# Performance work log

Measured on AMD Instinct MI355X. Metric: run time of the kernel, lower is better.

Reference implementation:

```python
import jax, jax.numpy as jnp
import numpy as np

B, S, D = 2, 2048, 1024
H = 16
DK = D // H  # 64
THETA = 10000.0
CLAMP = 80.0


def setup_inputs() -> dict:
    key = jax.random.key(0)
    ks = jax.random.split(key, 5)
    scale = 1.0 / np.sqrt(D)
    return {
        "x": jax.random.normal(ks[0], (B, S, D), jnp.float32),
        "Wq": jax.random.normal(ks[1], (D, D), jnp.float32) * scale,
        "Wk": jax.random.normal(ks[2], (D, D), jnp.float32) * scale,
        "Wv": jax.random.normal(ks[3], (D, D), jnp.float32) * scale,
        "Wo": jax.random.normal(ks[4], (D, D), jnp.float32) * scale,
    }


def _rope(x):
    # x: (B, H, S, DK); rotate interleaved even/odd pairs
    pos = jnp.arange(S, dtype=jnp.float32)  # token_positions = arange
    inv_freq = 1.0 / (THETA ** (jnp.arange(0, DK, 2, dtype=jnp.float32) / DK))
    ang = pos[:, None] * inv_freq[None, :]  # (S, DK/2)
    cos, sin = jnp.cos(ang), jnp.sin(ang)
    x1, x2 = x[..., 0::2], x[..., 1::2]
    r1 = x1 * cos - x2 * sin
    r2 = x1 * sin + x2 * cos
    out = jnp.stack([r1, r2], axis=-1).reshape(x.shape)
    return out


def reference(x, Wq, Wk, Wv, Wo):
    # fused-style QKV projections (bias-free Linear: y = x @ W^T)
    def proj(W):
        y = jnp.einsum('bsd,ed->bse', x, W)
        return y.reshape(B, S, H, DK).transpose(0, 2, 1, 3)  # b h s dk
    Q, K, V = proj(Wq), proj(Wk), proj(Wv)
    Q, K = _rope(Q), _rope(K)
    # naive attention with score clamp then causal mask then scaled softmax
    scores = jnp.einsum('bhqd,bhkd->bhqk', Q, K)
    scores = jnp.clip(scores, -CLAMP, CLAMP)
    causal = jnp.tril(jnp.ones((S, S), dtype=bool))  # (q, k)
    scores = jnp.where(causal, scores, -jnp.inf)
    weights = jax.nn.softmax(scores / np.sqrt(DK), axis=-1)
    att = jnp.einsum('bhqk,bhkd->bhqd', weights, V)
    att = att.transpose(0, 2, 1, 3).reshape(B, S, D)
    return jnp.einsum('bsd,ed->bse', att, Wo)
```

## Files before the change

### kernel.cpp

```cpp
#include <hip/hip_runtime.h>
#include <hip/hip_bf16.h>

#define Bc 2
#define Sc 2048
#define Dc 1024
#define Hc 16
#define DKc 64
#define Mrows 4096
#define QKV_LD 3072

typedef __bf16 bf16;
typedef __bf16 bf16x8 __attribute__((ext_vector_type(8)));
typedef __bf16 bf16x4 __attribute__((ext_vector_type(4)));
typedef float f32x4 __attribute__((ext_vector_type(4)));

__global__ void cvt_f32_bf16(const float* __restrict__ in, bf16* __restrict__ out, int n) {
    int idx = (blockIdx.x * blockDim.x + threadIdx.x) * 4;
    if (idx < n) {
        float4 v = *(const float4*)(in + idx);
        bf16x4 o = { (bf16)v.x, (bf16)v.y, (bf16)v.z, (bf16)v.w };
        *(bf16x4*)(out + idx) = o;
    }
}

__global__ void cvt_w4(const float* __restrict__ a, const float* __restrict__ b,
                       const float* __restrict__ c, const float* __restrict__ d,
                       bf16* __restrict__ oa, bf16* __restrict__ ob,
                       bf16* __restrict__ oc, bf16* __restrict__ od) {
    int idx = (blockIdx.x * blockDim.x + threadIdx.x) * 4;
    const float* in; bf16* out;
    switch (blockIdx.y) {
        case 0: in = a; out = oa; break;
        case 1: in = b; out = ob; break;
        case 2: in = c; out = oc; break;
        default: in = d; out = od; break;
    }
    float4 v = *(const float4*)(in + idx);
    bf16x4 o = { (bf16)v.x, (bf16)v.y, (bf16)v.z, (bf16)v.w };
    *(bf16x4*)(out + idx) = o;
}

__device__ __forceinline__ void gld_lds16(const bf16* g, bf16* l) {
    __builtin_amdgcn_global_load_lds((const __attribute__((address_space(1))) void*)g,
                                     (__attribute__((address_space(3))) void*)l, 16, 0, 0);
}

__device__ __forceinline__ unsigned bperm(int addrBytes, unsigned v) {
    return (unsigned)__builtin_amdgcn_ds_bpermute(addrBytes, (int)v);
}

template <typename OutT>
__global__ __launch_bounds__(512) void gemm_bt(const bf16* __restrict__ A,
                                               const bf16* __restrict__ Bt,
                                               OutT* __restrict__ C,
                                               int M, int N, int K) {
    __shared__ bf16 As[128 * 64];
    __shared__ bf16 Bs[128 * 64];
    const int tid = threadIdx.x;
    const int bm = blockIdx.y * 128, bn = blockIdx.x * 128;
    const int w = tid >> 6, l = tid & 63;
    const int wr = w >> 2, wc = w & 3;
    const int lr = l & 15, lc = l >> 4;

    const int srow = l >> 3;
    const int gl = (l & 7) ^ srow;
    const bf16* Ag = A  + (size_t)(bm + w * 16 + srow) * K + gl * 8;
    const bf16* Bg = Bt + (size_t)(bn + w * 16 + srow) * K + gl * 8;

    f32x4 acc[4][2] = {};

    for (int k0 = 0; k0 < K; k0 += 64) {
        __syncthreads();
#pragma unroll
        for (int c = 0; c < 2; c++) {
            gld_lds16(Ag + (size_t)(c * 8) * K + k0, &As[(w * 16 + c * 8) * 64]);
            gld_lds16(Bg + (size_t)(c * 8) * K + k0, &Bs[(w * 16 + c * 8) * 64]);
        }
        __syncthreads();
#pragma unroll
        for (int s = 0; s < 2; s++) {
            bf16x8 af[4], bfr[2];
#pragma unroll
            for (int i = 0; i < 4; i++) {
                const int R = wr * 64 + i * 16 + lr;
                af[i] = *(bf16x8*)&As[R * 64 + (((s * 4 + lc) ^ (R & 7)) * 8)];
            }
#pragma unroll
            for (int j = 0; j < 2; j++) {
                const int R = wc * 32 + j * 16 + lr;
                bfr[j] = *(bf16x8*)&Bs[R * 64 + (((s * 4 + lc) ^ (R & 7)) * 8)];
            }
#pragma unroll
            for (int i = 0; i < 4; i++)
#pragma unroll
                for (int j = 0; j < 2; j++)
                    acc[i][j] = __builtin_amdgcn_mfma_f32_16x16x32_bf16(af[i], bfr[j], acc[i][j], 0, 0, 0);
        }
    }

    const int cr = (l >> 4) * 4, cc = l & 15;
#pragma unroll
    for (int i = 0; i < 4; i++)
#pragma unroll
        for (int j = 0; j < 2; j++)
#pragma unroll
            for (int r = 0; r < 4; r++) {
                int row = bm + wr * 64 + i * 16 + cr + r;
                int col = bn + wc * 32 + j * 16 + cc;
                C[(size_t)row * N + col] = (OutT)acc[i][j][r];
            }
}

__global__ void rope_k(bf16* __restrict__ QKV) {
    int i = blockIdx.x * blockDim.x + threadIdx.x;
    int pair = i & 31;
    int h = (i >> 5) & 15;
    int s = (i >> 9) & 2047;
    int b = i >> 20;
    float inv_freq = exp2f(-0.41524101186f * (float)pair);
    float ang = (float)s * inv_freq;
    float c = cosf(ang), sn = sinf(ang);
    size_t base = ((size_t)(b * Sc + s)) * QKV_LD + h * 64 + pair * 2;
    float q1 = (float)QKV[base], q2 = (float)QKV[base + 1];
    QKV[base]     = (bf16)(q1 * c - q2 * sn);
    QKV[base + 1] = (bf16)(q1 * sn + q2 * c);
    size_t kb = base + 1024;
    float k1 = (float)QKV[kb], k2 = (float)QKV[kb + 1];
    QKV[kb]     = (bf16)(k1 * c - k2 * sn);
    QKV[kb + 1] = (bf16)(k1 * sn + k2 * c);
}

__global__ __launch_bounds__(256) void vtrans(const bf16* __restrict__ QKV, bf16* __restrict__ Vt) {
    __shared__ bf16 T[64 * 68];
    const int s0 = blockIdx.x * 64;
    const int bh = blockIdx.y;
    const int b = bh >> 4, h = bh & 15;
    const int tid = threadIdx.x;
    const bf16* src = QKV + (size_t)(b * Sc + s0) * QKV_LD + 2048 + h * 64;
#pragma unroll
    for (int p = 0; p < 2; p++) {
        int sr = (tid >> 3) + p * 32;
        int dk0 = (tid & 7) * 8;
        bf16x8 v = *(const bf16x8*)(src + (size_t)sr * QKV_LD + dk0);
        bf16x4 lo = { v[0], v[1], v[2], v[3] }, hi = { v[4], v[5], v[6], v[7] };
        *(bf16x4*)&T[sr * 68 + dk0]     = lo;
        *(bf16x4*)&T[sr * 68 + dk0 + 4] = hi;
    }
    __syncthreads();
    bf16* dst = Vt + (size_t)(bh * 64) * Sc + s0;
#pragma unroll
    for (int p = 0; p < 2; p++) {
        int dk = (tid >> 3) + p * 32;
        int sc0 = (tid & 7) * 8;
        bf16x8 v;
#pragma unroll
        for (int e = 0; e < 8; e++) v[e] = T[(sc0 + e) * 68 + dk];
        *(bf16x8*)(dst + (size_t)dk * Sc + sc0) = v;
    }
}

__global__ __launch_bounds__(256) void attn_k(const bf16* __restrict__ QKV,
                                              const bf16* __restrict__ Vt,
                                              bf16* __restrict__ Oa) {
    __shared__ bf16 Ks[2][64 * 64];
    __shared__ bf16 Vs[2][64 * 64];

    const int bid = blockIdx.x;
    const int qi = 31 - (bid >> 5);
    const int bh = bid & 31;
    const int h = bh & 15, b = bh >> 4;
    const int q0 = qi * 64;
    const int tid = threadIdx.x, w = tid >> 6, l = tid & 63;
    const int lr = l & 15, lc = l >> 4;

    const bf16* Qb  = QKV + (size_t)(b * Sc) * QKV_LD + h * 64;
    const bf16* Kb  = QKV + (size_t)(b * Sc) * QKV_LD + 1024 + h * 64;
    const bf16* Vtb = Vt + (size_t)(bh * 64) * Sc;

    const int qrow = q0 + w * 16 + lr;
    bf16x8 qf0 = *(const bf16x8*)(Qb + (size_t)qrow * QKV_LD + lc * 8);
    bf16x8 qf1 = *(const bf16x8*)(Qb + (size_t)qrow * QKV_LD + 32 + lc * 8);

    const int r8 = l >> 3, glg = (l & 7) ^ r8;
    const bf16* Kg = Kb  + (size_t)(16 * w + r8) * QKV_LD + glg * 8;
    const bf16* Vg = Vtb + (size_t)(16 * w + r8) * Sc + glg * 8;

    f32x4 oacc[4] = {};
    float psum = 0.f;

    const int sA = (lr + ((lc & 1) << 5)) << 2;
    const int sB = sA + (16 << 2);
    const bool hij = (lc & 2) != 0;

    const int nt = qi + 1;
    int cur = 0;

#define STAGE(T, BUF) {                                                            \
    const size_t kof = (size_t)((T) * 64) * QKV_LD;                                \
    const size_t vof = (size_t)((T) * 64);                                         \
    gld_lds16(Kg + kof,                    &Ks[BUF][(16 * w) * 64]);               \
    gld_lds16(Kg + kof + (size_t)8 * QKV_LD, &Ks[BUF][(16 * w + 8) * 64]);         \
    gld_lds16(Vg + vof,                    &Vs[BUF][(16 * w) * 64]);               \
    gld_lds16(Vg + vof + (size_t)8 * Sc,   &Vs[BUF][(16 * w + 8) * 64]); }

    STAGE(0, 0);
    for (int t = 0; t < nt; t++) {
        const int k0 = t * 64;
        if (t + 1 < nt) {
            __builtin_amdgcn_s_barrier();
            STAGE(t + 1, cur ^ 1);
            asm volatile("s_waitcnt vmcnt(4)" ::: "memory");
        } else {
            asm volatile("s_waitcnt vmcnt(0)" ::: "memory");
        }
        __builtin_amdgcn_s_barrier();

        f32x4 sfr[4];
#pragma unroll
        for (int j = 0; j < 4; j++) {
            const int R = j * 16 + lr;
            bf16x8 kf0 = *(bf16x8*)&Ks[cur][R * 64 + ((lc ^ (lr & 7)) * 8)];
            bf16x8 kf1 = *(bf16x8*)&Ks[cur][R * 64 + (((4 + lc) ^ (lr & 7)) * 8)];
            f32x4 z = {};
            z = __builtin_amdgcn_mfma_f32_16x16x32_bf16(kf0, qf0, z, 0, 0, 0);
            z = __builtin_amdgcn_mfma_f32_16x16x32_bf16(kf1, qf1, z, 0, 0, 0);
            sfr[j] = z;
        }

        const bool diag = (t == nt - 1);
        const int qg = q0 + w * 16 + lr;
        float pv[4][4];
#pragma unroll
        for (int j = 0; j < 4; j++)
#pragma unroll
            for (int r = 0; r < 4; r++) {
                float s = fminf(fmaxf(sfr[j][r], -80.f), 80.f);
                float p = __expf(s * 0.125f - 10.0f);
                if (diag && (k0 + j * 16 + lc * 4 + r) > qg) p = 0.f;
                psum += p;
                pv[j][r] = p;
            }

        unsigned pw0[4], pw1[4];
#pragma unroll
        for (int j = 0; j < 4; j++) {
            asm("v_cvt_pk_bf16_f32 %0, %1, %2" : "=v"(pw0[j]) : "v"(pv[j][0]), "v"(pv[j][1]));
            asm("v_cvt_pk_bf16_f32 %0, %1, %2" : "=v"(pw1[j]) : "v"(pv[j][2]), "v"(pv[j][3]));
        }

        union { int4 i; bf16x8 h; } u0, u1;
        {
            unsigned t0 = bperm(sA, pw0[0]), s0_ = bperm(sA, pw0[1]);
            unsigned t1 = bperm(sA, pw1[0]), s1_ = bperm(sA, pw1[1]);
            unsigned t2 = bperm(sB, pw0[0]), s2_ = bperm(sB, pw0[1]);
            unsigned t3 = bperm(sB, pw1[0]), s3_ = bperm(sB, pw1[1]);
            u0.i = (int4){ (int)(hij ? s0_ : t0), (int)(hij ? s1_ : t1),
                           (int)(hij ? s2_ : t2), (int)(hij ? s3_ : t3) };
            unsigned v0 = bperm(sA, pw0[2]), r0_ = bperm(sA, pw0[3]);
            unsigned v1 = bperm(sA, pw1[2]), r1_ = bperm(sA, pw1[3]);
            unsigned v2 = bperm(sB, pw0[2]), r2_ = bperm(sB, pw0[3]);
            unsigned v3 = bperm(sB, pw1[2]), r3_ = bperm(sB, pw1[3]);
            u1.i = (int4){ (int)(hij ? r0_ : v0), (int)(hij ? r1_ : v1),
                           (int)(hij ? r2_ : v2), (int)(hij ? r3_ : v3) };
        }

#pragma unroll
        for (int jd = 0; jd < 4; jd++) {
            const int R = jd * 16 + lr;
            bf16x8 vf0 = *(bf16x8*)&Vs[cur][R * 64 + ((lc ^ (lr & 7)) * 8)];
            bf16x8 vf1 = *(bf16x8*)&Vs[cur][R * 64 + (((4 + lc) ^ (lr & 7)) * 8)];
            oacc[jd] = __builtin_amdgcn_mfma_f32_16x16x32_bf16(u0.h, vf0, oacc[jd], 0, 0, 0);
            oacc[jd] = __builtin_amdgcn_mfma_f32_16x16x32_bf16(u1.h, vf1, oacc[jd], 0, 0, 0);
        }
        cur ^= 1;
    }

    psum += __shfl_xor(psum, 16, 64);
    psum += __shfl_xor(psum, 32, 64);
    float pr[4];
#pragma unroll
    for (int r = 0; r < 4; r++) pr[r] = __shfl(psum, lc * 4 + r, 64);

    bf16* Ob = Oa + (size_t)(b * Sc) * Dc + h * 64;
#pragma unroll
    for (int jd = 0; jd < 4; jd++)
#pragma unroll
        for (int r = 0; r < 4; r++) {
            int qg2 = q0 + w * 16 + lc * 4 + r;
            Ob[(size_t)qg2 * Dc + jd * 16 + lr] = (bf16)(oacc[jd][r] / pr[r]);
        }
#undef STAGE
}

extern "C" void kernel_launch(void* const* d_in, const int* in_sizes, int n_in,
                              void* d_out, int out_size, void* d_ws, size_t ws_size,
                              hipStream_t stream) {
    const float* x  = (const float*)d_in[0];
    const float* Wq = (const float*)d_in[1];
    const float* Wk = (const float*)d_in[2];
    const float* Wv = (const float*)d_in[3];
    const float* Wo = (const float*)d_in[4];

    const int NX = Bc * Sc * Dc;
    const int NW = Dc * Dc;

    bf16* xb   = (bf16*)d_ws;
    bf16* wqb  = xb + NX;
    bf16* wkb  = wqb + NW;
    bf16* wvb  = wkb + NW;
    bf16* wob  = wvb + NW;
    bf16* QKV  = wob + NW;
    bf16* Vt   = QKV + (size_t)Mrows * QKV_LD;
    bf16* att  = xb;

    cvt_f32_bf16<<<NX / 4 / 256, 256, 0, stream>>>(x, xb, NX);
    cvt_w4<<<dim3(NW / 4 / 256, 4), 256, 0, stream>>>(Wq, Wk, Wv, Wo, wqb, wkb, wvb, wob);

    gemm_bt<bf16><<<dim3(QKV_LD / 128, Mrows / 128), 512, 0, stream>>>(xb, wqb, QKV, Mrows, QKV_LD, Dc);

    rope_k<<<(Bc * Sc * Hc * 32) / 256, 256, 0, stream>>>(QKV);
    vtrans<<<dim3(Sc / 64, Bc * Hc), 256, 0, stream>>>(QKV, Vt);

    attn_k<<<Bc * Hc * (Sc / 64), 256, 0, stream>>>(QKV, Vt, att);

    gemm_bt<float><<<dim3(Dc / 128, Mrows / 128), 512, 0, stream>>>(att, wob, (float*)d_out, Mrows, Dc, Dc);
}
```

Baseline: 188.2 us.

## Pair high and low causal query tiles per block to balance attention work

Each attention block now handles two query tiles, tile p and tile 31-p, so every block does the same amount of causal work (33 KV tiles). KV tiles shared by both query tiles are loaded into LDS once and reused for both. The grid is halved to 512 blocks and each block holds two sets of accumulators, which raises register pressure and gives fewer blocks to hide latency with. The aim is to remove the load imbalance from the triangular causal mask and cut redundant K/V loads.

Result: slower. 197.4 us (+4.9%).

```diff
diff --git a/kernel.cpp b/kernel.cpp
--- a/kernel.cpp
+++ b/kernel.cpp
@@ -159,6 +159,88 @@
     }
 }
 
+__device__ __forceinline__ f32x4 mfma16(bf16x8 a, bf16x8 b, f32x4 c) {
+    return __builtin_amdgcn_mfma_f32_16x16x32_bf16(a, b, c, 0, 0, 0);
+}
+
+__device__ __forceinline__ void smax_exch(const f32x4* sfr, int k0, int qg, bool diag,
+                                          int lr, int lc, int sA, int sB, bool hij,
+                                          float& psum, bf16x8& a0, bf16x8& a1) {
+    float pv[4][4];
+#pragma unroll
+    for (int j = 0; j < 4; j++)
+#pragma unroll
+        for (int r = 0; r < 4; r++) {
+            float s = fminf(fmaxf(sfr[j][r], -80.f), 80.f);
+            float p = __expf(s * 0.125f - 10.0f);
+            if (diag && (k0 + j * 16 + lc * 4 + r) > qg) p = 0.f;
+            psum += p;
+            pv[j][r] = p;
+        }
+    unsigned pw0[4], pw1[4];
+#pragma unroll
+    for (int j = 0; j < 4; j++) {
+        asm("v_cvt_pk_bf16_f32 %0, %1, %2" : "=v"(pw0[j]) : "v"(pv[j][0]), "v"(pv[j][1]));
+        asm("v_cvt_pk_bf16_f32 %0, %1, %2" : "=v"(pw1[j]) : "v"(pv[j][2]), "v"(pv[j][3]));
+    }
+    union { int4 i; bf16x8 h; } u0, u1;
+    {
+        unsigned t0 = bperm(sA, pw0[0]), s0_ = bperm(sA, pw0[1]);
+        unsigned t1 = bperm(sA, pw1[0]), s1_ = bperm(sA, pw1[1]);
+        unsigned t2 = bperm(sB, pw0[0]), s2_ = bperm(sB, pw0[1]);
+        unsigned t3 = bperm(sB, pw1[0]), s3_ = bperm(sB, pw1[1]);
+        u0.i = (int4){ (int)(hij ? s0_ : t0), (int)(hij ? s1_ : t1),
+                       (int)(hij ? s2_ : t2), (int)(hij ? s3_ : t3) };
+        unsigned v0 = bperm(sA, pw0[2]), r0_ = bperm(sA, pw0[3]);
+        unsigned v1 = bperm(sA, pw1[2]), r1_ = bperm(sA, pw1[3]);
+        unsigned v2 = bperm(sB, pw0[2]), r2_ = bperm(sB, pw0[3]);
+        unsigned v3 = bperm(sB, pw1[2]), r3_ = bperm(sB, pw1[3]);
+        u1.i = (int4){ (int)(hij ? r0_ : v0), (int)(hij ? r1_ : v1),
+                       (int)(hij ? r2_ : v2), (int)(hij ? r3_ : v3) };
+    }
+    a0 = u0.h; a1 = u1.h;
+}
+
+template <bool DOL>
+__device__ __forceinline__ void attn_tile(const bf16* Ksb, const bf16* Vsb,
+                                          int lr, int lc, int k0,
+                                          bf16x8 qHf0, bf16x8 qHf1, bf16x8 qLf0, bf16x8 qLf1,
+                                          int qgH, int qgL, bool diagH, bool diagL,
+                                          int sA, int sB, bool hij,
+                                          f32x4* oH, f32x4* oL, float& psH, float& psL) {
+    f32x4 sH[4], sL[4];
+#pragma unroll
+    for (int j = 0; j < 4; j++) {
+        const int R = j * 16 + lr;
+        bf16x8 kf0 = *(bf16x8*)&Ksb[R * 64 + ((lc ^ (lr & 7)) * 8)];
+        bf16x8 kf1 = *(bf16x8*)&Ksb[R * 64 + (((4 + lc) ^ (lr & 7)) * 8)];
+        f32x4 z = {};
+        z = mfma16(kf0, qHf0, z); z = mfma16(kf1, qHf1, z);
+        sH[j] = z;
+        if constexpr (DOL) {
+            f32x4 y = {};
+            y = mfma16(kf0, qLf0, y); y = mfma16(kf1, qLf1, y);
+            sL[j] = y;
+        }
+    }
+    bf16x8 aH0, aH1, aL0, aL1;
+    smax_exch(sH, k0, qgH, diagH, lr, lc, sA, sB, hij, psH, aH0, aH1);
+    if constexpr (DOL) smax_exch(sL, k0, qgL, diagL, lr, lc, sA, sB, hij, psL, aL0, aL1);
+
+#pragma unroll
+    for (int jd = 0; jd < 4; jd++) {
+        const int R = jd * 16 + lr;
+        bf16x8 vf0 = *(bf16x8*)&Vsb[R * 64 + ((lc ^ (lr & 7)) * 8)];
+        bf16x8 vf1 = *(bf16x8*)&Vsb[R * 64 + (((4 + lc) ^ (lr & 7)) * 8)];
+        oH[jd] = mfma16(aH0, vf0, oH[jd]);
+        oH[jd] = mfma16(aH1, vf1, oH[jd]);
+        if constexpr (DOL) {
+            oL[jd] = mfma16(aL0, vf0, oL[jd]);
+            oL[jd] = mfma16(aL1, vf1, oL[jd]);
+        }
+    }
+}
+
 __global__ __launch_bounds__(256) void attn_k(const bf16* __restrict__ QKV,
                                               const bf16* __restrict__ Vt,
                                               bf16* __restrict__ Oa) {
@@ -166,10 +248,10 @@
     __shared__ bf16 Vs[2][64 * 64];
 
     const int bid = blockIdx.x;
-    const int qi = 31 - (bid >> 5);
+    const int p = bid >> 5;
     const int bh = bid & 31;
     const int h = bh & 15, b = bh >> 4;
-    const int q0 = qi * 64;
+    const int qHt = 31 - p, qLt = p;
     const int tid = threadIdx.x, w = tid >> 6, l = tid & 63;
     const int lr = l & 15, lc = l >> 4;
 
@@ -177,119 +259,99 @@
     const bf16* Kb  = QKV + (size_t)(b * Sc) * QKV_LD + 1024 + h * 64;
     const bf16* Vtb = Vt + (size_t)(bh * 64) * Sc;
 
-    const int qrow = q0 + w * 16 + lr;
-    bf16x8 qf0 = *(const bf16x8*)(Qb + (size_t)qrow * QKV_LD + lc * 8);
-    bf16x8 qf1 = *(const bf16x8*)(Qb + (size_t)qrow * QKV_LD + 32 + lc * 8);
+    const int qrowH = qHt * 64 + w * 16 + lr;
+    const int qrowL = qLt * 64 + w * 16 + lr;
+    bf16x8 qHf0 = *(const bf16x8*)(Qb + (size_t)qrowH * QKV_LD + lc * 8);
+    bf16x8 qHf1 = *(const bf16x8*)(Qb + (size_t)qrowH * QKV_LD + 32 + lc * 8);
+    bf16x8 qLf0 = *(const bf16x8*)(Qb + (size_t)qrowL * QKV_LD + lc * 8);
+    bf16x8 qLf1 = *(const bf16x8*)(Qb + (size_t)qrowL * QKV_LD + 32 + lc * 8);
 
     const int r8 = l >> 3, glg = (l & 7) ^ r8;
     const bf16* Kg = Kb  + (size_t)(16 * w + r8) * QKV_LD + glg * 8;
     const bf16* Vg = Vtb + (size_t)(16 * w + r8) * Sc + glg * 8;
 
-    f32x4 oacc[4] = {};
-    float psum = 0.f;
+    f32x4 oH[4] = {}, oL[4] = {};
+    float psH = 0.f, psL = 0.f;
 
     const int sA = (lr + ((lc & 1) << 5)) << 2;
     const int sB = sA + (16 << 2);
     const bool hij = (lc & 2) != 0;
 
-    const int nt = qi + 1;
+    const int qgH = qHt * 64 + w * 16 + lr;
+    const int qgL = qLt * 64 + w * 16 + lr;
+
+    const int nt = qHt + 1;
     int cur = 0;
 
 #define STAGE(T, BUF) {                                                            \
     const size_t kof = (size_t)((T) * 64) * QKV_LD;                                \
     const size_t vof = (size_t)((T) * 64);                                         \
-    gld_lds16(Kg + kof,                    &Ks[BUF][(16 * w) * 64]);               \
+    gld_lds16(Kg + kof,                      &Ks[BUF][(16 * w) * 64]);             \
     gld_lds16(Kg + kof + (size_t)8 * QKV_LD, &Ks[BUF][(16 * w + 8) * 64]);         \
-    gld_lds16(Vg + vof,                    &Vs[BUF][(16 * w) * 64]);               \
-    gld_lds16(Vg + vof + (size_t)8 * Sc,   &Vs[BUF][(16 * w + 8) * 64]); }
+    gld_lds16(Vg + vof,                      &Vs[BUF][(16 * w) * 64]);             \
+    gld_lds16(Vg + vof + (size_t)8 * Sc,     &Vs[BUF][(16 * w + 8) * 64]); }
 
     STAGE(0, 0);
-    for (int t = 0; t < nt; t++) {
-        const int k0 = t * 64;
+    for (int t = 0; t <= p; t++) {
+        __builtin_amdgcn_s_barrier();
+        STAGE(t + 1, cur ^ 1);
+        asm volatile("s_waitcnt vmcnt(4)" ::: "memory");
+        __builtin_amdgcn_sched_barrier(0);
+        __builtin_amdgcn_s_barrier();
+        attn_tile<true>(Ks[cur], Vs[cur], lr, lc, t * 64,
+                        qHf0, qHf1, qLf0, qLf1, qgH, qgL,
+                        false, (t == p), sA, sB, hij, oH, oL, psH, psL);
+        cur ^= 1;
+    }
+    for (int t = p + 1; t < nt; t++) {
         if (t + 1 < nt) {
             __builtin_amdgcn_s_barrier();
             STAGE(t + 1, cur ^ 1);
             asm volatile("s_waitcnt vmcnt(4)" ::: "memory");
+            __builtin_amdgcn_sched_barrier(0);
         } else {
             asm volatile("s_waitcnt vmcnt(0)" ::: "memory");
+            __builtin_amdgcn_sched_barrier(0);
         }
         __builtin_amdgcn_s_barrier();
-
-        f32x4 sfr[4];
-#pragma unroll
-        for (int j = 0; j < 4; j++) {
-            const int R = j * 16 + lr;
-            bf16x8 kf0 = *(bf16x8*)&Ks[cur][R * 64 + ((lc ^ (lr & 7)) * 8)];
-            bf16x8 kf1 = *(bf16x8*)&Ks[cur][R * 64 + (((4 + lc) ^ (lr & 7)) * 8)];
-            f32x4 z = {};
-            z = __builtin_amdgcn_mfma_f32_16x16x32_bf16(kf0, qf0, z, 0, 0, 0);
-            z = __builtin_amdgcn_mfma_f32_16x16x32_bf16(kf1, qf1, z, 0, 0, 0);
-            sfr[j] = z;
-        }
-
-        const bool diag = (t == nt - 1);
-        const int qg = q0 + w * 16 + lr;
-        float pv[4][4];
-#pragma unroll
-        for (int j = 0; j < 4; j++)
+        attn_tile<false>(Ks[cur], Vs[cur], lr, lc, t * 64,
+                         qHf0, qHf1, qLf0, qLf1, qgH, qgL,
+                         (t == nt - 1), false, sA, sB, hij, oH, oL, psH, psL);
+        cur ^= 1;
+    }
+#undef STAGE
+
+    bf16* Ob = Oa + (size_t)(b * Sc) * Dc + h * 64;
+    {
+        float ps = psH;
+        ps += __shfl_xor(ps, 16, 64);
+        ps += __shfl_xor(ps, 32, 64);
+        float pr[4];
+#pragma unroll
+        for (int r = 0; r < 4; r++) pr[r] = __shfl(ps, lc * 4 + r, 64);
+#pragma unroll
+        for (int jd = 0; jd < 4; jd++)
 #pragma unroll
             for (int r = 0; r < 4; r++) {
-                float s = fminf(fmaxf(sfr[j][r], -80.f), 80.f);
-                float p = __expf(s * 0.125f - 10.0f);
-                if (diag && (k0 + j * 16 + lc * 4 + r) > qg) p = 0.f;
-                psum += p;
-                pv[j][r] = p;
-            }
-
-        unsigned pw0[4], pw1[4];
-#pragma unroll
-        for (int j = 0; j < 4; j++) {
-            asm("v_cvt_pk_bf16_f32 %0, %1, %2" : "=v"(pw0[j]) : "v"(pv[j][0]), "v"(pv[j][1]));
-            asm("v_cvt_pk_bf16_f32 %0, %1, %2" : "=v"(pw1[j]) : "v"(pv[j][2]), "v"(pv[j][3]));
-        }
-
-        union { int4 i; bf16x8 h; } u0, u1;
-        {
-            unsigned t0 = bperm(sA, pw0[0]), s0_ = bperm(sA, pw0[1]);
-            unsigned t1 = bperm(sA, pw1[0]), s1_ = bperm(sA, pw1[1]);
-            unsigned t2 = bperm(sB, pw0[0]), s2_ = bperm(sB, pw0[1]);
-            unsigned t3 = bperm(sB, pw1[0]), s3_ = bperm(sB, pw1[1]);
-            u0.i = (int4){ (int)(hij ? s0_ : t0), (int)(hij ? s1_ : t1),
-                           (int)(hij ? s2_ : t2), (int)(hij ? s3_ : t3) };
-            unsigned v0 = bperm(sA, pw0[2]), r0_ = bperm(sA, pw0[3]);
-            unsigned v1 = bperm(sA, pw1[2]), r1_ = bperm(sA, pw1[3]);
-            unsigned v2 = bperm(sB, pw0[2]), r2_ = bperm(sB, pw0[3]);
-            unsigned v3 = bperm(sB, pw1[2]), r3_ = bperm(sB, pw1[3]);
-            u1.i = (int4){ (int)(hij ? r0_ : v0), (int)(hij ? r1_ : v1),
-                           (int)(hij ? r2_ : v2), (int)(hij ? r3_ : v3) };
-        }
-
-#pragma unroll
-        for (int jd = 0; jd < 4; jd++) {
-            const int R = jd * 16 + lr;
-            bf16x8 vf0 = *(bf16x8*)&Vs[cur][R * 64 + ((lc ^ (lr & 7)) * 8)];
-            bf16x8 vf1 = *(bf16x8*)&Vs[cur][R * 64 + (((4 + lc) ^ (lr & 7)) * 8)];
-            oacc[jd] = __builtin_amdgcn_mfma_f32_16x16x32_bf16(u0.h, vf0, oacc[jd], 0, 0, 0);
-            oacc[jd] = __builtin_amdgcn_mfma_f32_16x16x32_bf16(u1.h, vf1, oacc[jd], 0, 0, 0);
-        }
-        cur ^= 1;
-    }
-
-    psum += __shfl_xor(psum, 16, 64);
-    psum += __shfl_xor(psum, 32, 64);
-    float pr[4];
-#pragma unroll
-    for (int r = 0; r < 4; r++) pr[r] = __shfl(psum, lc * 4 + r, 64);
-
-    bf16* Ob = Oa + (size_t)(b * Sc) * Dc + h * 64;
-#pragma unroll
-    for (int jd = 0; jd < 4; jd++)
-#pragma unroll
-        for (int r = 0; r < 4; r++) {
-            int qg2 = q0 + w * 16 + lc * 4 + r;
-            Ob[(size_t)qg2 * Dc + jd * 16 + lr] = (bf16)(oacc[jd][r] / pr[r]);
-        }
-#undef STAGE
+                int qg2 = qHt * 64 + w * 16 + lc * 4 + r;
+                Ob[(size_t)qg2 * Dc + jd * 16 + lr] = (bf16)(oH[jd][r] / pr[r]);
+            }
+    }
+    {
+        float ps = psL;
+        ps += __shfl_xor(ps, 16, 64);
+        ps += __shfl_xor(ps, 32, 64);
+        float pr[4];
+#pragma unroll
+        for (int r = 0; r < 4; r++) pr[r] = __shfl(ps, lc * 4 + r, 64);
+#pragma unroll
+        for (int jd = 0; jd < 4; jd++)
+#pragma unroll
+            for (int r = 0; r < 4; r++) {
+                int qg2 = qLt * 64 + w * 16 + lc * 4 + r;
+                Ob[(size_t)qg2 * Dc + jd * 16 + lr] = (bf16)(oL[jd][r] / pr[r]);
+            }
+    }
 }
 
 extern "C" void kernel_launch(void* const* d_in, const int* in_sizes, int n_in,
@@ -321,7 +383,7 @@
     rope_k<<<(Bc * Sc * Hc * 32) / 256, 256, 0, stream>>>(QKV);
     vtrans<<<dim3(Sc / 64, Bc * Hc), 256, 0, stream>>>(QKV, Vt);
 
-    attn_k<<<Bc * Hc * (Sc / 64), 256, 0, stream>>>(QKV, Vt, att);
+    attn_k<<<16 * Bc * Hc, 256, 0, stream>>>(QKV, Vt, att);
 
     gemm_bt<float><<<dim3(Dc / 128, Mrows / 128), 512, 0, stream>>>(att, wob, (float*)d_out, Mrows, Dc, Dc);
 }
```

## Split attention KV loop across two wave groups with LDS reduction

Applied to the files above, without the earlier changes.

The attention kernel now launches 512 threads per block. Two groups of four waves each take alternate KV tiles for the same 64 query rows, each with its own double-buffered LDS staging. At the end, group 1 writes its partial output accumulators and row sums to LDS and group 0 adds them before normalising and storing. This halves the serial KV loop length per block and adds waves to hide latency, at the cost of doubled LDS use, a final cross-group reduction and possible idle waves on odd tile counts.

Result: no change. 187.6 us (-0.3%).

```diff
diff --git a/kernel.cpp b/kernel.cpp
--- a/kernel.cpp
+++ b/kernel.cpp
@@ -159,11 +159,52 @@
     }
 }
 
-__global__ __launch_bounds__(256) void attn_k(const bf16* __restrict__ QKV,
+__device__ __forceinline__ f32x4 mfma16(bf16x8 a, bf16x8 b, f32x4 c) {
+    return __builtin_amdgcn_mfma_f32_16x16x32_bf16(a, b, c, 0, 0, 0);
+}
+
+__device__ __forceinline__ void smax_exch(const f32x4* sfr, int k0, int qg, bool diag,
+                                          int lr, int lc, int sA, int sB, bool hij,
+                                          float& psum, bf16x8& a0, bf16x8& a1) {
+    float pv[4][4];
+#pragma unroll
+    for (int j = 0; j < 4; j++)
+#pragma unroll
+        for (int r = 0; r < 4; r++) {
+            float s = fminf(fmaxf(sfr[j][r], -80.f), 80.f);
+            float p = __expf(s * 0.125f - 10.0f);
+            if (diag && (k0 + j * 16 + lc * 4 + r) > qg) p = 0.f;
+            psum += p;
+            pv[j][r] = p;
+        }
+    unsigned pw0[4], pw1[4];
+#pragma unroll
+    for (int j = 0; j < 4; j++) {
+        asm("v_cvt_pk_bf16_f32 %0, %1, %2" : "=v"(pw0[j]) : "v"(pv[j][0]), "v"(pv[j][1]));
+        asm("v_cvt_pk_bf16_f32 %0, %1, %2" : "=v"(pw1[j]) : "v"(pv[j][2]), "v"(pv[j][3]));
+    }
+    union { int4 i; bf16x8 h; } u0, u1;
+    {
+        unsigned t0 = bperm(sA, pw0[0]), s0_ = bperm(sA, pw0[1]);
+        unsigned t1 = bperm(sA, pw1[0]), s1_ = bperm(sA, pw1[1]);
+        unsigned t2 = bperm(sB, pw0[0]), s2_ = bperm(sB, pw0[1]);
+        unsigned t3 = bperm(sB, pw1[0]), s3_ = bperm(sB, pw1[1]);
+        u0.i = (int4){ (int)(hij ? s0_ : t0), (int)(hij ? s1_ : t1),
+                       (int)(hij ? s2_ : t2), (int)(hij ? s3_ : t3) };
+        unsigned v0 = bperm(sA, pw0[2]), r0_ = bperm(sA, pw0[3]);
+        unsigned v1 = bperm(sA, pw1[2]), r1_ = bperm(sA, pw1[3]);
+        unsigned v2 = bperm(sB, pw0[2]), r2_ = bperm(sB, pw0[3]);
+        unsigned v3 = bperm(sB, pw1[2]), r3_ = bperm(sB, pw1[3]);
+        u1.i = (int4){ (int)(hij ? r0_ : v0), (int)(hij ? r1_ : v1),
+                       (int)(hij ? r2_ : v2), (int)(hij ? r3_ : v3) };
+    }
+    a0 = u0.h; a1 = u1.h;
+}
+
+__global__ __launch_bounds__(512) void attn_k(const bf16* __restrict__ QKV,
                                               const bf16* __restrict__ Vt,
                                               bf16* __restrict__ Oa) {
-    __shared__ bf16 Ks[2][64 * 64];
-    __shared__ bf16 Vs[2][64 * 64];
+    __shared__ bf16 KV[2][2][2][64 * 64];
 
     const int bid = blockIdx.x;
     const int qi = 31 - (bid >> 5);
@@ -171,125 +212,116 @@
     const int h = bh & 15, b = bh >> 4;
     const int q0 = qi * 64;
     const int tid = threadIdx.x, w = tid >> 6, l = tid & 63;
+    const int g = w >> 2, w4 = w & 3;
     const int lr = l & 15, lc = l >> 4;
 
     const bf16* Qb  = QKV + (size_t)(b * Sc) * QKV_LD + h * 64;
-    const bf16* Kb  = QKV + (size_t)(b * Sc) * QKV_LD + 1024 + h * 64;
+    const bf16* Kb  = Qb + 1024;
     const bf16* Vtb = Vt + (size_t)(bh * 64) * Sc;
 
-    const int qrow = q0 + w * 16 + lr;
+    const int qrow = q0 + w4 * 16 + lr;
     bf16x8 qf0 = *(const bf16x8*)(Qb + (size_t)qrow * QKV_LD + lc * 8);
     bf16x8 qf1 = *(const bf16x8*)(Qb + (size_t)qrow * QKV_LD + 32 + lc * 8);
 
     const int r8 = l >> 3, glg = (l & 7) ^ r8;
-    const bf16* Kg = Kb  + (size_t)(16 * w + r8) * QKV_LD + glg * 8;
-    const bf16* Vg = Vtb + (size_t)(16 * w + r8) * Sc + glg * 8;
+    const bf16* Kg = Kb  + (size_t)(16 * w4 + r8) * QKV_LD + glg * 8;
+    const bf16* Vg = Vtb + (size_t)(16 * w4 + r8) * Sc + glg * 8;
 
     f32x4 oacc[4] = {};
     float psum = 0.f;
 
     const int sA = (lr + ((lc & 1) << 5)) << 2;
-    const int sB = sA + (16 << 2);
+    const int sB = sA + 64;
     const bool hij = (lc & 2) != 0;
+    const int qg = q0 + w4 * 16 + lr;
 
     const int nt = qi + 1;
-    int cur = 0;
+    const int nit = (nt + 1) >> 1;
 
 #define STAGE(T, BUF) {                                                            \
     const size_t kof = (size_t)((T) * 64) * QKV_LD;                                \
     const size_t vof = (size_t)((T) * 64);                                         \
-    gld_lds16(Kg + kof,                    &Ks[BUF][(16 * w) * 64]);               \
-    gld_lds16(Kg + kof + (size_t)8 * QKV_LD, &Ks[BUF][(16 * w + 8) * 64]);         \
-    gld_lds16(Vg + vof,                    &Vs[BUF][(16 * w) * 64]);               \
-    gld_lds16(Vg + vof + (size_t)8 * Sc,   &Vs[BUF][(16 * w + 8) * 64]); }
-
-    STAGE(0, 0);
-    for (int t = 0; t < nt; t++) {
-        const int k0 = t * 64;
-        if (t + 1 < nt) {
-            __builtin_amdgcn_s_barrier();
-            STAGE(t + 1, cur ^ 1);
+    gld_lds16(Kg + kof,                      &KV[g][BUF][0][(16 * w4) * 64]);      \
+    gld_lds16(Kg + kof + (size_t)8 * QKV_LD, &KV[g][BUF][0][(16 * w4 + 8) * 64]);  \
+    gld_lds16(Vg + vof,                      &KV[g][BUF][1][(16 * w4) * 64]);      \
+    gld_lds16(Vg + vof + (size_t)8 * Sc,     &KV[g][BUF][1][(16 * w4 + 8) * 64]); }
+
+    if (g < nt) STAGE(g, 0);
+    int buf = 0;
+    for (int i = 0; i < nit; i++) {
+        const int t = 2 * i + g;
+        __builtin_amdgcn_s_barrier();
+        if (t + 2 < nt) {
+            STAGE(t + 2, buf ^ 1);
             asm volatile("s_waitcnt vmcnt(4)" ::: "memory");
         } else {
             asm volatile("s_waitcnt vmcnt(0)" ::: "memory");
         }
+        __builtin_amdgcn_sched_barrier(0);
         __builtin_amdgcn_s_barrier();
 
-        f32x4 sfr[4];
-#pragma unroll
-        for (int j = 0; j < 4; j++) {
-            const int R = j * 16 + lr;
-            bf16x8 kf0 = *(bf16x8*)&Ks[cur][R * 64 + ((lc ^ (lr & 7)) * 8)];
-            bf16x8 kf1 = *(bf16x8*)&Ks[cur][R * 64 + (((4 + lc) ^ (lr & 7)) * 8)];
-            f32x4 z = {};
-            z = __builtin_amdgcn_mfma_f32_16x16x32_bf16(kf0, qf0, z, 0, 0, 0);
-            z = __builtin_amdgcn_mfma_f32_16x16x32_bf16(kf1, qf1, z, 0, 0, 0);
-            sfr[j] = z;
-        }
-
-        const bool diag = (t == nt - 1);
-        const int qg = q0 + w * 16 + lr;
-        float pv[4][4];
-#pragma unroll
-        for (int j = 0; j < 4; j++)
+        if (t < nt) {
+            const bf16* Ksb = KV[g][buf][0];
+            const bf16* Vsb = KV[g][buf][1];
+            f32x4 sfr[4];
+#pragma unroll
+            for (int j = 0; j < 4; j++) {
+                const int R = j * 16 + lr;
+                bf16x8 kf0 = *(bf16x8*)&Ksb[R * 64 + ((lc ^ (lr & 7)) * 8)];
+                bf16x8 kf1 = *(bf16x8*)&Ksb[R * 64 + (((4 + lc) ^ (lr & 7)) * 8)];
+                f32x4 z = {};
+                z = mfma16(kf0, qf0, z);
+                z = mfma16(kf1, qf1, z);
+                sfr[j] = z;
+            }
+            bf16x8 a0, a1;
+            smax_exch(sfr, t * 64, qg, (t == nt - 1), lr, lc, sA, sB, hij, psum, a0, a1);
+#pragma unroll
+            for (int jd = 0; jd < 4; jd++) {
+                const int R = jd * 16 + lr;
+                bf16x8 vf0 = *(bf16x8*)&Vsb[R * 64 + ((lc ^ (lr & 7)) * 8)];
+                bf16x8 vf1 = *(bf16x8*)&Vsb[R * 64 + (((4 + lc) ^ (lr & 7)) * 8)];
+                oacc[jd] = mfma16(a0, vf0, oacc[jd]);
+                oacc[jd] = mfma16(a1, vf1, oacc[jd]);
+            }
+        }
+        buf ^= 1;
+    }
+#undef STAGE
+
+    __builtin_amdgcn_s_barrier();
+    float* F = (float*)&KV[0][0][0][0];
+    const int ci = (w4 * 64 + l) * 17;
+    if (g == 1) {
+#pragma unroll
+        for (int jd = 0; jd < 4; jd++)
+#pragma unroll
+            for (int r = 0; r < 4; r++) F[ci + jd * 4 + r] = oacc[jd][r];
+        F[ci + 16] = psum;
+    }
+    __builtin_amdgcn_s_barrier();
+    if (g == 0) {
+#pragma unroll
+        for (int jd = 0; jd < 4; jd++)
+#pragma unroll
+            for (int r = 0; r < 4; r++) oacc[jd][r] += F[ci + jd * 4 + r];
+        psum += F[ci + 16];
+
+        psum += __shfl_xor(psum, 16, 64);
+        psum += __shfl_xor(psum, 32, 64);
+        float pr[4];
+#pragma unroll
+        for (int r = 0; r < 4; r++) pr[r] = __shfl(psum, lc * 4 + r, 64);
+
+        bf16* Ob = Oa + (size_t)(b * Sc) * Dc + h * 64;
+#pragma unroll
+        for (int jd = 0; jd < 4; jd++)
 #pragma unroll
             for (int r = 0; r < 4; r++) {
-                float s = fminf(fmaxf(sfr[j][r], -80.f), 80.f);
-                float p = __expf(s * 0.125f - 10.0f);
-                if (diag && (k0 + j * 16 + lc * 4 + r) > qg) p = 0.f;
-                psum += p;
-                pv[j][r] = p;
-            }
-
-        unsigned pw0[4], pw1[4];
-#pragma unroll
-        for (int j = 0; j < 4; j++) {
-            asm("v_cvt_pk_bf16_f32 %0, %1, %2" : "=v"(pw0[j]) : "v"(pv[j][0]), "v"(pv[j][1]));
-            asm("v_cvt_pk_bf16_f32 %0, %1, %2" : "=v"(pw1[j]) : "v"(pv[j][2]), "v"(pv[j][3]));
-        }
-
-        union { int4 i; bf16x8 h; } u0, u1;
-        {
-            unsigned t0 = bperm(sA, pw0[0]), s0_ = bperm(sA, pw0[1]);
-            unsigned t1 = bperm(sA, pw1[0]), s1_ = bperm(sA, pw1[1]);
-            unsigned t2 = bperm(sB, pw0[0]), s2_ = bperm(sB, pw0[1]);
-            unsigned t3 = bperm(sB, pw1[0]), s3_ = bperm(sB, pw1[1]);
-            u0.i = (int4){ (int)(hij ? s0_ : t0), (int)(hij ? s1_ : t1),
-                           (int)(hij ? s2_ : t2), (int)(hij ? s3_ : t3) };
-            unsigned v0 = bperm(sA, pw0[2]), r0_ = bperm(sA, pw0[3]);
-            unsigned v1 = bperm(sA, pw1[2]), r1_ = bperm(sA, pw1[3]);
-            unsigned v2 = bperm(sB, pw0[2]), r2_ = bperm(sB, pw0[3]);
-            unsigned v3 = bperm(sB, pw1[2]), r3_ = bperm(sB, pw1[3]);
-            u1.i = (int4){ (int)(hij ? r0_ : v0), (int)(hij ? r1_ : v1),
-                           (int)(hij ? r2_ : v2), (int)(hij ? r3_ : v3) };
-        }
-
-#pragma unroll
-        for (int jd = 0; jd < 4; jd++) {
-            const int R = jd * 16 + lr;
-            bf16x8 vf0 = *(bf16x8*)&Vs[cur][R * 64 + ((lc ^ (lr & 7)) * 8)];
-            bf16x8 vf1 = *(bf16x8*)&Vs[cur][R * 64 + (((4 + lc) ^ (lr & 7)) * 8)];
-            oacc[jd] = __builtin_amdgcn_mfma_f32_16x16x32_bf16(u0.h, vf0, oacc[jd], 0, 0, 0);
-            oacc[jd] = __builtin_amdgcn_mfma_f32_16x16x32_bf16(u1.h, vf1, oacc[jd], 0, 0, 0);
-        }
-        cur ^= 1;
-    }
-
-    psum += __shfl_xor(psum, 16, 64);
-    psum += __shfl_xor(psum, 32, 64);
-    float pr[4];
-#pragma unroll
-    for (int r = 0; r < 4; r++) pr[r] = __shfl(psum, lc * 4 + r, 64);
-
-    bf16* Ob = Oa + (size_t)(b * Sc) * Dc + h * 64;
-#pragma unroll
-    for (int jd = 0; jd < 4; jd++)
-#pragma unroll
-        for (int r = 0; r < 4; r++) {
-            int qg2 = q0 + w * 16 + lc * 4 + r;
-            Ob[(size_t)qg2 * Dc + jd * 16 + lr] = (bf16)(oacc[jd][r] / pr[r]);
-        }
-#undef STAGE
+                int qg2 = q0 + w4 * 16 + lc * 4 + r;
+                Ob[(size_t)qg2 * Dc + jd * 16 + lr] = (bf16)(oacc[jd][r] / pr[r]);
+            }
+    }
 }
 
 extern "C" void kernel_launch(void* const* d_in, const int* in_sizes, int n_in,
@@ -321,7 +353,7 @@
     rope_k<<<(Bc * Sc * Hc * 32) / 256, 256, 0, stream>>>(QKV);
     vtrans<<<dim3(Sc / 64, Bc * Hc), 256, 0, stream>>>(QKV, Vt);
 
-    attn_k<<<Bc * Hc * (Sc / 64), 256, 0, stream>>>(QKV, Vt, att);
+    attn_k<<<Bc * Hc * (Sc / 64), 512, 0, stream>>>(QKV, Vt, att);
 
     gemm_bt<float><<<dim3(Dc / 128, Mrows / 128), 512, 0, stream>>>(att, wob, (float*)d_out, Mrows, Dc, Dc);
 }
```
